# Kernel tuning notes

Hardware: AMD Instinct MI355X
Metric: run time of the kernel (lower is better)

The kernel has to match this reference:

```python
import jax, jax.numpy as jnp
import numpy as np

N = 100000   # nodes
E = 800000   # edges
IN = 128     # in_dim
H = 256      # hidden
G = 512      # global cache rows


def _w(k, shape):
    fan_in = shape[0]
    return jax.random.normal(k, shape, jnp.float32) / np.sqrt(fan_in)


def setup_inputs() -> dict:
    key = jax.random.key(0)
    ks = jax.random.split(key, 24)
    x = jax.random.normal(ks[0], (N, IN), jnp.float32)
    edge_index = jax.random.randint(ks[1], (2, E), 0, N, jnp.int64)
    global_cache = jax.random.normal(ks[2], (G, H), jnp.float32)
    return {
        "x": x,
        "edge_index": edge_index,
        "global_cache": global_cache,
        "Wp": _w(ks[3], (IN, 64)), "bp": jnp.zeros((64,), jnp.float32),
        "W1l": _w(ks[4], (64, H)), "b1l": jnp.zeros((H,), jnp.float32),
        "W1r": _w(ks[5], (64, H)),
        "W2l": _w(ks[6], (H, H)), "b2l": jnp.zeros((H,), jnp.float32),
        "W2r": _w(ks[7], (H, H)),
        "Wq": _w(ks[8], (H, H)), "bq": jnp.zeros((H,), jnp.float32),
        "Wk": _w(ks[9], (H, H)), "bk": jnp.zeros((H,), jnp.float32),
        "Wv": _w(ks[10], (H, H)), "bv": jnp.zeros((H,), jnp.float32),
        "Wm1": _w(ks[11], (2 * H, H)), "bm1": jnp.zeros((H,), jnp.float32),
        "Wm2": _w(ks[12], (H, 2)), "bm2": jnp.zeros((2,), jnp.float32),
    }


def _sage(h, src, dst, Wl, bl, Wr):
    # PyG SAGEConv (mean aggr): lin_l(mean_{j in N(i)} h_j) + lin_r(h_i)
    agg = jax.ops.segment_sum(h[src], dst, num_segments=N)          # [N, d]
    cnt = jax.ops.segment_sum(jnp.ones((src.shape[0],), h.dtype), dst, num_segments=N)
    mean = agg / jnp.maximum(cnt, 1.0)[:, None]
    return mean @ Wl + bl + h @ Wr


def reference(x, edge_index, global_cache, Wp, bp, W1l, b1l, W1r,
              W2l, b2l, W2r, Wq, bq, Wk, bk, Wv, bv, Wm1, bm1, Wm2, bm2):
    src, dst = edge_index[0], edge_index[1]
    x_emb = jax.nn.relu(x @ Wp + bp)                                 # [N, 64]
    h = jax.nn.relu(_sage(x_emb, src, dst, W1l, b1l, W1r))           # [N, H]
    # dropout is identity in eval mode
    h = _sage(h, src, dst, W2l, b2l, W2r)                            # [N, H]
    # global attention
    Q = h @ Wq + bq                                                  # [N, H]
    K = global_cache @ Wk + bk                                       # [G, H]
    V = global_cache @ Wv + bv                                       # [G, H]
    attn = jax.nn.softmax(Q @ K.T / np.sqrt(H).astype(np.float32), axis=-1)  # [N, G]
    g = attn @ V                                                     # [N, H]
    h_cat = jnp.concatenate([h, g], axis=1)                          # [N, 2H]
    out = jax.nn.relu(h_cat @ Wm1 + bm1) @ Wm2 + bm2                 # [N, 2]
    return out
```

## Files before the change

### kernel.cpp

```cpp
#include <hip/hip_runtime.h>
#include <cstdint>
#include <cstddef>


#define NN 100000
#define NE 800000
#define CR 100000
#define NB1 98
#define CNTB 3125
#define XCVB 12500
#define NJOB 11
#define WCVB (NJOB * 32)
#define EMB_MB 782

typedef __attribute__((ext_vector_type(8))) short short8;
typedef __attribute__((ext_vector_type(8))) unsigned short ushort8;
typedef __attribute__((ext_vector_type(4))) float f32x4;

__device__ __forceinline__ float b2f(ushort u) {
  union { unsigned u; float f; } v; v.u = ((unsigned)u) << 16; return v.f;
}
__device__ __forceinline__ ushort f2b(float f) {
  union { float f; unsigned u; } v; v.f = f;
  unsigned r = v.u + 0x7FFFu + ((v.u >> 16) & 1u);
  return (ushort)(r >> 16);
}
__device__ __forceinline__ void gl_lds16(const void* g, void* l) {
  __builtin_amdgcn_global_load_lds((const __attribute__((address_space(1))) void*)g,
                                   (__attribute__((address_space(3))) void*)l, 16, 0, 0);
}

__global__ void zero_detect_k(const int* __restrict__ ei, int* __restrict__ flag,
                              int* __restrict__ cnt, int n) {
  if (blockIdx.x == 0) {
    __shared__ int ok;
    int t = threadIdx.x;
    if (t == 0) ok = 1;
    __syncthreads();
    if (ei[2 * t + 1] != 0) ok = 0;
    __syncthreads();
    if (t == 0) *flag = ok;
  } else {
    int i = (blockIdx.x - 1) * 256 + threadIdx.x;
    if (i < n) cnt[i] = 0;
  }
}

struct CvtJobs {
  const float* src[NJOB];
  ushort* dst[NJOB];
  int R[NJOB], C[NJOB], off[NJOB], tr[NJOB];
  float sc[NJOB];
};

__global__ void count_cvt_k(const int* __restrict__ ei, const int* __restrict__ flag,
                            int* __restrict__ cnt, int* __restrict__ loc,
                            const float* __restrict__ x, ushort* __restrict__ xb,
                            int E, int n4, CvtJobs jb) {
  int b = blockIdx.x;
  if (b < CNTB + XCVB) {
    int q = b / 5;
    if (b - q * 5 == 0) {
      int i = q * 256 + threadIdx.x;
      if (i >= E) return;
      const bool i64 = (*flag != 0);
      unsigned d = (unsigned)(i64 ? ei[2 * E + 2 * i] : ei[E + i]);
      int p = -1;
      if (d < NN) p = atomicAdd(&cnt[d], 1);
      loc[i] = p;
    } else {
      int i = (b - q - 1) * 256 + threadIdx.x;
      if (i < n4) {
        float4 v = ((const float4*)x)[i];
        ushort4 o; o.x = f2b(v.x); o.y = f2b(v.y); o.z = f2b(v.z); o.w = f2b(v.w);
        ((ushort4*)xb)[i] = o;
      }
    }
  } else {
    int wb = b - CNTB - XCVB;
    int j = wb >> 5;
    int ib = wb & 31;
    const int Cj = jb.C[j], Rj = jb.R[j];
    const float sc = jb.sc[j];
    const int n = Rj * Cj;
    if (jb.tr[j]) {
      for (int i = ib * 256 + threadIdx.x; i < n; i += 32 * 256) {
        int c = i / Rj, r = i - c * Rj;
        jb.dst[j][i] = f2b(jb.src[j][(size_t)(jb.off[j] + r) * Cj + c] * sc);
      }
    } else {
      for (int i = ib * 256 + threadIdx.x; i < n; i += 32 * 256)
        jb.dst[j][i] = f2b(jb.src[j][i] * sc);
    }
  }
}

__device__ __forceinline__ void scan1_body(const int* __restrict__ cnt,
                                           int* __restrict__ rowptr,
                                           int* __restrict__ bsum, int n, int b,
                                           char* smem) {
  int* ls = (int*)smem;
  const int t = threadIdx.x;
  const int base = b * 1024 + t * 4;
  int v[4]; int s = 0;
#pragma unroll
  for (int j = 0; j < 4; ++j) { int i = base + j; v[j] = (i < n) ? cnt[i] : 0; s += v[j]; }
  ls[t] = s; __syncthreads();
  int x = s;
  for (int o = 1; o < 256; o <<= 1) {
    int a = (t >= o) ? ls[t - o] : 0; __syncthreads();
    x += a; ls[t] = x; __syncthreads();
  }
  int run = x - s;
#pragma unroll
  for (int j = 0; j < 4; ++j) { run += v[j]; int i = base + j; if (i < n) rowptr[i + 1] = run; }
  if (t == 255) bsum[b] = x;
}

__device__ __forceinline__ void scan2_body(const int* __restrict__ bsum,
                                           int* __restrict__ boff, int nb,
                                           char* smem) {
  int* ls = (int*)smem;
  int t = threadIdx.x;
  int v = (t < 128 && t < nb) ? bsum[t] : 0;
  if (t < 128) ls[t] = v;
  __syncthreads();
  int x = v;
  for (int o = 1; o < 128; o <<= 1) {
    int a = (t < 128 && t >= o) ? ls[t - o] : 0;
    __syncthreads();
    x += a;
    if (t < 128) ls[t] = x;
    __syncthreads();
  }
  if (t < 128 && t < nb) boff[t] = x - v;
}

__device__ __forceinline__ void sbias_body(const float* __restrict__ bq,
                                           const ushort* __restrict__ Kmat,
                                           float* __restrict__ sbias, int blk) {
  int g = blk * 4 + (threadIdx.x >> 6);
  int lane = threadIdx.x & 63;
  if (g >= 512) return;
  ushort4 kv = ((const ushort4*)(Kmat + (size_t)g * 256))[lane];
  float4 bv = ((const float4*)bq)[lane];
  float p = b2f(kv.x) * bv.x + b2f(kv.y) * bv.y + b2f(kv.z) * bv.z + b2f(kv.w) * bv.w;
  for (int off = 32; off; off >>= 1) p += __shfl_xor(p, off);
  if (lane == 0) sbias[g] = p * 0.0625f;
}

__global__ void scan3_k(int* __restrict__ rowptr, const int* __restrict__ boff, int n) {
  int i = blockIdx.x * 256 + threadIdx.x;
  if (i == 0) rowptr[0] = 0;
  if (i < n) rowptr[i + 1] += boff[i >> 10];
}

__global__ void fill_edges_k(const int* __restrict__ ei, const int* __restrict__ flag,
                             const int* __restrict__ rowptr, const int* __restrict__ loc,
                             int* __restrict__ eidx, int E) {
  int i = blockIdx.x * 256 + threadIdx.x;
  if (i >= E) return;
  const bool i64 = (*flag != 0);
  unsigned s = (unsigned)(i64 ? ei[2 * i] : ei[i]);
  unsigned d = (unsigned)(i64 ? ei[2 * E + 2 * i] : ei[E + i]);
  int lc = loc[i];
  if (d < NN && s < NN && lc >= 0) {
    unsigned p = (unsigned)(rowptr[d] + lc);
    if (p < (unsigned)E) eidx[p] = (int)s;
  }
}

__global__ void agg64_k(const ushort* __restrict__ X, const int* __restrict__ rowptr,
                        const int* __restrict__ eidx, ushort* __restrict__ mean,
                        int r0, int M) {
  int nl = blockIdx.x * 4 + (threadIdx.x >> 6);
  int l = threadIdx.x & 63;
  int e4 = l >> 4;
  int d4 = l & 15;
  if (nl >= M) return;
  int node = r0 + nl;
  int s = rowptr[node], e = rowptr[node + 1];
  float a0 = 0.f, a1 = 0.f, a2 = 0.f, a3 = 0.f;
  for (int i = s + e4; i < e; i += 4) {
    unsigned sc = (unsigned)eidx[i];
    if (sc < NN) {
      ushort4 v = ((const ushort4*)(X + (size_t)sc * 64))[d4];
      a0 += b2f(v.x); a1 += b2f(v.y); a2 += b2f(v.z); a3 += b2f(v.w);
    }
  }
  a0 += __shfl_xor(a0, 16); a0 += __shfl_xor(a0, 32);
  a1 += __shfl_xor(a1, 16); a1 += __shfl_xor(a1, 32);
  a2 += __shfl_xor(a2, 16); a2 += __shfl_xor(a2, 32);
  a3 += __shfl_xor(a3, 16); a3 += __shfl_xor(a3, 32);
  if (e4 == 0) {
    float inv = 1.f / (float)max(e - s, 1);
    ushort4 o; o.x = f2b(a0 * inv); o.y = f2b(a1 * inv); o.z = f2b(a2 * inv); o.w = f2b(a3 * inv);
    ((ushort4*)(mean + (size_t)nl * 64))[d4] = o;
  }
}

__global__ void agg256_k(const ushort* __restrict__ X, const int* __restrict__ rowptr,
                         const int* __restrict__ eidx, ushort* __restrict__ mean,
                         int r0, int M) {
  int nl = blockIdx.x * 4 + (threadIdx.x >> 6);
  int l = threadIdx.x & 63;
  int g = l >> 5;
  int d = l & 31;
  if (nl >= M) return;
  int node = r0 + nl;
  int s = rowptr[node], e = rowptr[node + 1];
  float a[8], c[8];
#pragma unroll
  for (int k = 0; k < 8; ++k) { a[k] = 0.f; c[k] = 0.f; }
  for (int i = s + g; i < e; i += 4) {
    unsigned s0 = (unsigned)eidx[i];
    if (s0 < NN) {
      ushort8 v = *(const ushort8*)(X + (size_t)s0 * 256 + d * 8);
#pragma unroll
      for (int k = 0; k < 8; ++k) a[k] += b2f((ushort)v[k]);
    }
    int i2 = i + 2;
    if (i2 < e) {
      unsigned s1 = (unsigned)eidx[i2];
      if (s1 < NN) {
        ushort8 v = *(const ushort8*)(X + (size_t)s1 * 256 + d * 8);
#pragma unroll
        for (int k = 0; k < 8; ++k) c[k] += b2f((ushort)v[k]);
      }
    }
  }
  float inv = 1.f / (float)max(e - s, 1);
  ushort8 o;
#pragma unroll
  for (int k = 0; k < 8; ++k) {
    float t = a[k] + c[k];
    t += __shfl_xor(t, 32);
    o[k] = (short)f2b(t * inv);
  }
  if (g == 0) *(ushort8*)(mean + (size_t)nl * 256 + d * 8) = o;
}

template<int BN, bool RELU, bool OUTBF>
__device__ __forceinline__ void gemm_body(
    const ushort* __restrict__ A1, const ushort* __restrict__ BT1, int K1,
    const ushort* __restrict__ A2, const ushort* __restrict__ BT2, int K2,
    const float* __restrict__ bias, void* __restrict__ Cv, int M, int Nc,
    int bmi, int bni, char* smem) {
  constexpr int NR = BN / 32;
  constexpr int WTN = BN / 2;
  constexpr int ABYT = 128 * 64 * 2;
  constexpr int BBYT = BN * 64 * 2;
  constexpr int BUF = ABYT + BBYT;
  constexpr int CP = BN + 8;
  const int tid = threadIdx.x;
  const int l = tid & 63;
  const int w = tid >> 6;
  const int wm = w >> 1, wn = w & 1;
  const int bm = bmi * 128, bn = bni * BN;
  const int r15 = l & 15, g4 = l >> 4;

  const int nt1 = K1 >> 6;
  const int nt2 = A2 ? (K2 >> 6) : 0;
  const int nt = nt1 + nt2;

  auto STAGE = [&](int buf, int t) {
    const ushort* A = (t < nt1) ? A1 : A2;
    const ushort* BT = (t < nt1) ? BT1 : BT2;
    const int K = (t < nt1) ? K1 : K2;
    const int k0 = ((t < nt1) ? t : t - nt1) << 6;
    char* As = smem + buf * BUF;
    char* Bs = As + ABYT;
#pragma unroll
    for (int p = 0; p < 4; ++p) {
      int idx = tid + p * 256;
      int row = idx >> 3, slot = idx & 7;
      int kb = slot ^ (row & 7);
      int grow = bm + row; if (grow >= M) grow = M - 1;
      gl_lds16(A + (size_t)grow * K + k0 + kb * 8, As + idx * 16);
    }
#pragma unroll
    for (int p = 0; p < BN / 32; ++p) {
      int idx = tid + p * 256;
      int row = idx >> 3, slot = idx & 7;
      int kb = slot ^ (row & 7);
      gl_lds16(BT + (size_t)(bn + row) * K + k0 + kb * 8, Bs + idx * 16);
    }
  };

  f32x4 acc[4][NR];
  const f32x4 zz = {0.f, 0.f, 0.f, 0.f};
#pragma unroll
  for (int m = 0; m < 4; ++m)
#pragma unroll
    for (int n = 0; n < NR; ++n) acc[m][n] = zz;

  STAGE(0, 0);
  int cur = 0;
  for (int t = 0; t < nt; ++t) {
    __syncthreads();
    if (t + 1 < nt) STAGE(cur ^ 1, t + 1);
    const char* As = smem + cur * BUF;
    const char* Bs = As + ABYT;
#pragma unroll
    for (int s = 0; s < 2; ++s) {
      short8 a[4], b[NR];
      const int slotx = (((s * 4 + g4) ^ (r15 & 7)) << 4);
#pragma unroll
      for (int m = 0; m < 4; ++m) {
        int row = wm * 64 + m * 16 + r15;
        a[m] = *(const short8*)(As + row * 128 + slotx);
      }
#pragma unroll
      for (int n = 0; n < NR; ++n) {
        int row = wn * WTN + n * 16 + r15;
        b[n] = *(const short8*)(Bs + row * 128 + slotx);
      }
#pragma unroll
      for (int m = 0; m < 4; ++m)
#pragma unroll
        for (int n = 0; n < NR; ++n)
          acc[m][n] = __builtin_amdgcn_mfma_f32_16x16x32_bf16(a[m], b[n], acc[m][n], 0, 0, 0);
    }
    cur ^= 1;
  }
  __syncthreads();
  if (OUTBF) {
    ushort* Cs = (ushort*)smem;
#pragma unroll
    for (int n = 0; n < NR; ++n) {
      int col = wn * WTN + n * 16 + r15;
      float bv = bias ? bias[bn + col] : 0.f;
#pragma unroll
      for (int m = 0; m < 4; ++m) {
#pragma unroll
        for (int j = 0; j < 4; ++j) {
          int row = wm * 64 + m * 16 + g4 * 4 + j;
          float v = acc[m][n][j] + bv;
          if (RELU) v = fmaxf(v, 0.f);
          Cs[row * CP + col] = f2b(v);
        }
      }
    }
    __syncthreads();
    constexpr int C8 = BN / 8;
    for (int it = tid; it < 128 * C8; it += 256) {
      int row = it / C8, c8 = it % C8;
      if (bm + row < M)
        *(ushort8*)((ushort*)Cv + (size_t)(bm + row) * Nc + bn + c8 * 8) =
            *(const ushort8*)(Cs + row * CP + c8 * 8);
    }
  } else {
#pragma unroll
    for (int n = 0; n < NR; ++n) {
      int col = bn + wn * WTN + n * 16 + r15;
      float bv = bias ? bias[col] : 0.f;
#pragma unroll
      for (int m = 0; m < 4; ++m) {
#pragma unroll
        for (int j = 0; j < 4; ++j) {
          int row = bm + wm * 64 + m * 16 + g4 * 4 + j;
          if (row < M) {
            float v = acc[m][n][j] + bv;
            if (RELU) v = fmaxf(v, 0.f);
            ((float*)Cv)[(size_t)row * Nc + col] = v;
          }
        }
      }
    }
  }
}

template<bool RELU>
__global__ __launch_bounds__(256)
void gemm64_k(const ushort* __restrict__ A1, const ushort* __restrict__ BT1, int K1,
              const ushort* __restrict__ A2, const ushort* __restrict__ BT2, int K2,
              const float* __restrict__ bias, ushort* __restrict__ C, int M, int Nc) {
  constexpr int NR = 8;
  constexpr int WTN = 128;
  constexpr int ABYT = 64 * 32 * 2;
  constexpr int BBYT = 256 * 32 * 2;
  constexpr int BUF = ABYT + BBYT;
  constexpr int CP = 256 + 8;
  __shared__ __align__(16) char smem[2 * BUF];
  const int tid = threadIdx.x;
  const int l = tid & 63;
  const int w = tid >> 6;
  const int wm = w >> 1, wn = w & 1;
  const int bm = blockIdx.x * 64;
  const int bn = blockIdx.y * 256;
  const int r15 = l & 15, g4 = l >> 4;

  const int nt1 = K1 >> 5;
  const int nt2 = A2 ? (K2 >> 5) : 0;
  const int nt = nt1 + nt2;

  auto STAGE = [&](int buf, int t) {
    const ushort* A = (t < nt1) ? A1 : A2;
    const ushort* BT = (t < nt1) ? BT1 : BT2;
    const int K = (t < nt1) ? K1 : K2;
    const int k0 = ((t < nt1) ? t : t - nt1) << 5;
    char* As = smem + buf * BUF;
    char* Bs = As + ABYT;
    {
      int row = tid >> 2, slot = tid & 3;
      int kb = slot ^ ((row >> 1) & 3);
      int grow = bm + row; if (grow >= M) grow = M - 1;
      gl_lds16(A + (size_t)grow * K + k0 + kb * 8, As + tid * 16);
    }
#pragma unroll
    for (int p = 0; p < 4; ++p) {
      int idx = tid + p * 256;
      int row = idx >> 2, slot = idx & 3;
      int kb = slot ^ ((row >> 1) & 3);
      gl_lds16(BT + (size_t)(bn + row) * K + k0 + kb * 8, Bs + idx * 16);
    }
  };

  f32x4 acc[2][NR];
  const f32x4 zz = {0.f, 0.f, 0.f, 0.f};
#pragma unroll
  for (int m = 0; m < 2; ++m)
#pragma unroll
    for (int n = 0; n < NR; ++n) acc[m][n] = zz;

  STAGE(0, 0);
  int cur = 0;
  for (int t = 0; t < nt; ++t) {
    __syncthreads();
    if (t + 1 < nt) STAGE(cur ^ 1, t + 1);
    const char* As = smem + cur * BUF;
    const char* Bs = As + ABYT;
    short8 a[2], b[NR];
#pragma unroll
    for (int m = 0; m < 2; ++m) {
      int row = wm * 32 + m * 16 + r15;
      a[m] = *(const short8*)(As + row * 64 + ((g4 ^ ((row >> 1) & 3)) << 4));
    }
#pragma unroll
    for (int n = 0; n < NR; ++n) {
      int row = wn * WTN + n * 16 + r15;
      b[n] = *(const short8*)(Bs + row * 64 + ((g4 ^ ((row >> 1) & 3)) << 4));
    }
#pragma unroll
    for (int m = 0; m < 2; ++m)
#pragma unroll
      for (int n = 0; n < NR; ++n)
        acc[m][n] = __builtin_amdgcn_mfma_f32_16x16x32_bf16(a[m], b[n], acc[m][n], 0, 0, 0);
    cur ^= 1;
  }
  __syncthreads();
  ushort* Cs = (ushort*)smem;
#pragma unroll
  for (int n = 0; n < NR; ++n) {
    int col = wn * WTN + n * 16 + r15;
    float bv = bias ? bias[bn + col] : 0.f;
#pragma unroll
    for (int m = 0; m < 2; ++m) {
#pragma unroll
      for (int j = 0; j < 4; ++j) {
        int row = wm * 32 + m * 16 + g4 * 4 + j;
        float v = acc[m][n][j] + bv;
        if (RELU) v = fmaxf(v, 0.f);
        Cs[row * CP + col] = f2b(v);
      }
    }
  }
  __syncthreads();
  for (int it = tid; it < 64 * 32; it += 256) {
    int row = it >> 5, c8 = it & 31;
    if (bm + row < M)
      *(ushort8*)(C + (size_t)(bm + row) * Nc + bn + c8 * 8) =
          *(const ushort8*)(Cs + row * CP + c8 * 8);
  }
}

__global__ __launch_bounds__(256)
void stage2_k(const int* __restrict__ cnt, int* __restrict__ rowptr, int* __restrict__ bsum,
              const ushort* __restrict__ gcb, const ushort* __restrict__ WkT,
              const float* __restrict__ bk, ushort* __restrict__ Kmatb,
              const ushort* __restrict__ WvT, const float* __restrict__ bvv,
              ushort* __restrict__ Vmatb,
              const ushort* __restrict__ xb, const ushort* __restrict__ WpT,
              const float* __restrict__ bp, ushort* __restrict__ x_emb) {
  __shared__ __align__(16) char smem[65536];
  int b = blockIdx.x;
  if (b < 8) {
    gemm_body<128, false, true>(gcb, WkT, 256, nullptr, nullptr, 0, bk, Kmatb,
                                512, 256, b & 3, b >> 2, smem);
  } else if (b < 16) {
    int lb = b - 8;
    gemm_body<128, false, true>(gcb, WvT, 256, nullptr, nullptr, 0, bvv, Vmatb,
                                512, 256, lb & 3, lb >> 2, smem);
  } else if (b < 16 + EMB_MB) {
    gemm_body<64, true, true>(xb, WpT, 128, nullptr, nullptr, 0, bp, x_emb,
                              NN, 64, b - 16, 0, smem);
  } else {
    scan1_body(cnt, rowptr, bsum, NN, b - (16 + EMB_MB), smem);
  }
}

__global__ __launch_bounds__(256)
void stage3_k(const ushort* __restrict__ Kmatb, const ushort* __restrict__ Wqb,
              ushort* __restrict__ KWqT,
              const ushort* __restrict__ Wm1bT, const ushort* __restrict__ Vmatb,
              ushort* __restrict__ W_pvT,
              const float* __restrict__ bq, float* __restrict__ sbias,
              const int* __restrict__ bsum, int* __restrict__ boff) {
  __shared__ __align__(16) char smem[65536];
  int b = blockIdx.x;
  if (b < 8) {
    gemm_body<128, false, true>(Kmatb, Wqb, 256, nullptr, nullptr, 0, nullptr, KWqT,
                                512, 256, b & 3, b >> 2, smem);
  } else if (b < 16) {
    int lb = b - 8;
    gemm_body<128, false, true>(Wm1bT, Vmatb, 256, nullptr, nullptr, 0, nullptr, W_pvT,
                                256, 512, lb & 1, lb >> 1, smem);
  } else if (b < 144) {
    sbias_body(bq, Kmatb, sbias, b - 16);
  } else {
    scan2_body(bsum, boff, NB1, smem);
  }
}

__global__ __launch_bounds__(256)
void mlp_out_k(const ushort* __restrict__ A1, const ushort* __restrict__ BT1, int K1,
               const ushort* __restrict__ A2, const ushort* __restrict__ BT2, int K2,
               const float* __restrict__ bias, const float* __restrict__ Wm2,
               const float* __restrict__ bm2, float* __restrict__ out, int M) {
  constexpr int NR = 8;
  constexpr int WTN = 128;
  constexpr int ABYT = 64 * 32 * 2;
  constexpr int BBYT = 256 * 32 * 2;
  constexpr int BUF = ABYT + BBYT;
  __shared__ __align__(16) char smem[2 * BUF];
  const int tid = threadIdx.x;
  const int l = tid & 63;
  const int w = tid >> 6;
  const int wm = w >> 1, wn = w & 1;
  const int bm = blockIdx.x * 64;
  const int r15 = l & 15, g4 = l >> 4;

  const int nt1 = K1 >> 5;
  const int nt2 = K2 >> 5;
  const int nt = nt1 + nt2;

  auto STAGE = [&](int buf, int t) {
    const ushort* A = (t < nt1) ? A1 : A2;
    const ushort* BT = (t < nt1) ? BT1 : BT2;
    const int K = (t < nt1) ? K1 : K2;
    const int k0 = ((t < nt1) ? t : t - nt1) << 5;
    char* As = smem + buf * BUF;
    char* Bs = As + ABYT;
    {
      int row = tid >> 2, slot = tid & 3;
      int kb = slot ^ ((row >> 1) & 3);
      int grow = bm + row; if (grow >= M) grow = M - 1;
      gl_lds16(A + (size_t)grow * K + k0 + kb * 8, As + tid * 16);
    }
#pragma unroll
    for (int p = 0; p < 4; ++p) {
      int idx = tid + p * 256;
      int row = idx >> 2, slot = idx & 3;
      int kb = slot ^ ((row >> 1) & 3);
      gl_lds16(BT + (size_t)row * K + k0 + kb * 8, Bs + idx * 16);
    }
  };

  f32x4 acc[2][NR];
  const f32x4 zz = {0.f, 0.f, 0.f, 0.f};
#pragma unroll
  for (int m = 0; m < 2; ++m)
#pragma unroll
    for (int n = 0; n < NR; ++n) acc[m][n] = zz;

  STAGE(0, 0);
  int cur = 0;
  for (int t = 0; t < nt; ++t) {
    __syncthreads();
    if (t + 1 < nt) STAGE(cur ^ 1, t + 1);
    const char* As = smem + cur * BUF;
    const char* Bs = As + ABYT;
    short8 a[2], b[NR];
#pragma unroll
    for (int m = 0; m < 2; ++m) {
      int row = wm * 32 + m * 16 + r15;
      a[m] = *(const short8*)(As + row * 64 + ((g4 ^ ((row >> 1) & 3)) << 4));
    }
#pragma unroll
    for (int n = 0; n < NR; ++n) {
      int row = wn * WTN + n * 16 + r15;
      b[n] = *(const short8*)(Bs + row * 64 + ((g4 ^ ((row >> 1) & 3)) << 4));
    }
#pragma unroll
    for (int m = 0; m < 2; ++m)
#pragma unroll
      for (int n = 0; n < NR; ++n)
        acc[m][n] = __builtin_amdgcn_mfma_f32_16x16x32_bf16(a[m], b[n], acc[m][n], 0, 0, 0);
    cur ^= 1;
  }
  __syncthreads();
  float bv[NR], w20[NR], w21[NR];
#pragma unroll
  for (int n = 0; n < NR; ++n) {
    int col = wn * WTN + n * 16 + r15;
    bv[n] = bias[col];
    w20[n] = Wm2[col * 2 + 0];
    w21[n] = Wm2[col * 2 + 1];
  }
  float* red = (float*)smem;
#pragma unroll
  for (int m = 0; m < 2; ++m) {
#pragma unroll
    for (int j = 0; j < 4; ++j) {
      float p0 = 0.f, p1 = 0.f;
#pragma unroll
      for (int n = 0; n < NR; ++n) {
        float v = fmaxf(acc[m][n][j] + bv[n], 0.f);
        p0 += v * w20[n];
        p1 += v * w21[n];
      }
      p0 += __shfl_xor(p0, 1); p1 += __shfl_xor(p1, 1);
      p0 += __shfl_xor(p0, 2); p1 += __shfl_xor(p1, 2);
      p0 += __shfl_xor(p0, 4); p1 += __shfl_xor(p1, 4);
      p0 += __shfl_xor(p0, 8); p1 += __shfl_xor(p1, 8);
      if (r15 == 0) {
        int rl = wm * 32 + m * 16 + g4 * 4 + j;
        red[wn * 128 + rl * 2 + 0] = p0;
        red[wn * 128 + rl * 2 + 1] = p1;
      }
    }
  }
  __syncthreads();
  if (tid < 128) {
    int rl = tid >> 1, j = tid & 1;
    int row = bm + rl;
    if (row < M)
      out[(size_t)row * 2 + j] = red[rl * 2 + j] + red[128 + rl * 2 + j] + bm2[j];
  }
}

__global__ void softmax_k(ushort* __restrict__ SP, int M) {
  int row = blockIdx.x * 4 + (threadIdx.x >> 6);
  int lane = threadIdx.x & 63;
  if (row >= M) return;
  ushort4* p = (ushort4*)(SP + (size_t)row * 512);
  ushort4 ua = p[lane];
  ushort4 ub = p[lane + 64];
  float ax = b2f(ua.x), ay = b2f(ua.y), az = b2f(ua.z), aw = b2f(ua.w);
  float bx = b2f(ub.x), by = b2f(ub.y), bz = b2f(ub.z), bw = b2f(ub.w);
  float m = fmaxf(fmaxf(fmaxf(ax, ay), fmaxf(az, aw)),
                  fmaxf(fmaxf(bx, by), fmaxf(bz, bw)));
  for (int off = 32; off; off >>= 1) m = fmaxf(m, __shfl_xor(m, off));
  ax = expf(ax - m); ay = expf(ay - m); az = expf(az - m); aw = expf(aw - m);
  bx = expf(bx - m); by = expf(by - m); bz = expf(bz - m); bw = expf(bw - m);
  float s = ax + ay + az + aw + bx + by + bz + bw;
  for (int off = 32; off; off >>= 1) s += __shfl_xor(s, off);
  float inv = 1.f / s;
  ushort4 oa, ob;
  oa.x = f2b(ax * inv); oa.y = f2b(ay * inv); oa.z = f2b(az * inv); oa.w = f2b(aw * inv);
  ob.x = f2b(bx * inv); ob.y = f2b(by * inv); ob.z = f2b(bz * inv); ob.w = f2b(bw * inv);
  p[lane] = oa;
  p[lane + 64] = ob;
}

extern "C" void kernel_launch(void* const* d_in, const int* in_sizes, int n_in,
                              void* d_out, int out_size, void* d_ws, size_t ws_size,
                              hipStream_t stream) {
  const int N = NN, E = NE;
  const float* x   = (const float*)d_in[0];
  const int*   ei  = (const int*)d_in[1];
  const float* gc  = (const float*)d_in[2];
  const float* Wp  = (const float*)d_in[3];
  const float* bp  = (const float*)d_in[4];
  const float* W1l = (const float*)d_in[5];
  const float* b1l = (const float*)d_in[6];
  const float* W1r = (const float*)d_in[7];
  const float* W2l = (const float*)d_in[8];
  const float* b2l = (const float*)d_in[9];
  const float* W2r = (const float*)d_in[10];
  const float* Wq  = (const float*)d_in[11];
  const float* bq  = (const float*)d_in[12];
  const float* Wk  = (const float*)d_in[13];
  const float* bk  = (const float*)d_in[14];
  const float* Wv  = (const float*)d_in[15];
  const float* bv  = (const float*)d_in[16];
  const float* Wm1 = (const float*)d_in[17];
  const float* bm1 = (const float*)d_in[18];
  const float* Wm2 = (const float*)d_in[19];
  const float* bm2 = (const float*)d_in[20];
  float* out = (float*)d_out;

  char* base = (char*)d_ws;
  size_t off = 0;
  auto take = [&](size_t bytes) -> void* {
    void* r = base + off;
    off += (bytes + 255) & ~(size_t)255;
    return r;
  };
  int* cnt    = (int*)take((size_t)N * 4);
  int* rowptr = (int*)take((size_t)(N + 1) * 4);
  int* loc    = (int*)take((size_t)E * 4);
  int* eidx   = (int*)take((size_t)E * 4);
  int* eflag  = (int*)take(256);
  int* bsum   = (int*)take(NB1 * 4);
  int* boff   = (int*)take(NB1 * 4);
  ushort* WpT   = (ushort*)take((size_t)64 * 128 * 2);
  ushort* W1lT  = (ushort*)take((size_t)256 * 64 * 2);
  ushort* W1rT  = (ushort*)take((size_t)256 * 64 * 2);
  ushort* W2lT  = (ushort*)take((size_t)256 * 256 * 2);
  ushort* W2rT  = (ushort*)take((size_t)256 * 256 * 2);
  ushort* WkT   = (ushort*)take((size_t)256 * 256 * 2);
  ushort* WvT   = (ushort*)take((size_t)256 * 256 * 2);
  ushort* Wqb   = (ushort*)take((size_t)256 * 256 * 2);
  ushort* Wm1aT = (ushort*)take((size_t)256 * 256 * 2);
  ushort* Wm1bT = (ushort*)take((size_t)256 * 256 * 2);
  ushort* gcb   = (ushort*)take((size_t)512 * 256 * 2);
  ushort* Kmatb = (ushort*)take((size_t)512 * 256 * 2);
  ushort* Vmatb = (ushort*)take((size_t)512 * 256 * 2);
  ushort* W_pvT = (ushort*)take((size_t)256 * 512 * 2);
  ushort* KWqT  = (ushort*)take((size_t)512 * 256 * 2);
  float*  sbias = (float*)take((size_t)512 * 4);
  char* U = (char*)take((size_t)N * 1536);
  ushort* h = (ushort*)take((size_t)N * 256 * 2);
  if (off > ws_size) return;

  ushort* xb    = (ushort*)U;
  ushort* x_emb = (ushort*)(U + (size_t)N * 256);
  ushort* mean1 = (ushort*)(U + (size_t)N * 384);
  ushort* h2_c     = (ushort*)U;
  ushort* SP_c     = (ushort*)(U + (size_t)N * 512);
  ushort* mean2_c  = SP_c;

  const int n4 = N * 128 / 4;
  dim3 thr(256);

  CvtJobs jb;
  {
    const float* s_[NJOB] = {gc, Wq, Wp, W1l, W1r, W2l, W2r, Wk, Wv, Wm1, Wm1};
    ushort* d_[NJOB] = {gcb, Wqb, WpT, W1lT, W1rT, W2lT, W2rT, WkT, WvT, Wm1aT, Wm1bT};
    int R_[NJOB] = {512, 256, 128, 64, 64, 256, 256, 256, 256, 256, 256};
    int C_[NJOB] = {256, 256, 64, 256, 256, 256, 256, 256, 256, 256, 256};
    int o_[NJOB] = {0, 0, 0, 0, 0, 0, 0, 0, 0, 0, 256};
    int t_[NJOB] = {0, 0, 1, 1, 1, 1, 1, 1, 1, 1, 1};
    for (int j = 0; j < NJOB; ++j) {
      jb.src[j] = s_[j]; jb.dst[j] = d_[j]; jb.R[j] = R_[j]; jb.C[j] = C_[j];
      jb.off[j] = o_[j]; jb.tr[j] = t_[j]; jb.sc[j] = (j == 1) ? 0.0625f : 1.0f;
    }
  }

  zero_detect_k<<<1 + (N + 255) / 256, thr, 0, stream>>>(ei, eflag, cnt, N);
  count_cvt_k<<<CNTB + XCVB + WCVB, thr, 0, stream>>>(ei, eflag, cnt, loc, x, xb, E, n4, jb);
  stage2_k<<<16 + EMB_MB + NB1, thr, 0, stream>>>(
      cnt, rowptr, bsum, gcb, WkT, bk, Kmatb, WvT, bv, Vmatb, xb, WpT, bp, x_emb);
  stage3_k<<<145, thr, 0, stream>>>(
      Kmatb, Wqb, KWqT, Wm1bT, Vmatb, W_pvT, bq, sbias, bsum, boff);
  scan3_k<<<(N + 255) / 256, thr, 0, stream>>>(rowptr, boff, N);
  fill_edges_k<<<(E + 255) / 256, thr, 0, stream>>>(ei, eflag, rowptr, loc, eidx, E);

  agg64_k<<<(N + 3) / 4, thr, 0, stream>>>(x_emb, rowptr, eidx, mean1, 0, N);
  gemm64_k<true><<<dim3((N + 63) / 64, 1), thr, 0, stream>>>(
      mean1, W1lT, 64, x_emb, W1rT, 64, b1l, h, N, 256);

  {
    const int CRc = N;
    const int MBc64 = (CRc + 63) / 64;
    agg256_k<<<(CRc + 3) / 4, thr, 0, stream>>>(h, rowptr, eidx, mean2_c, 0, CRc);
    gemm64_k<false><<<dim3(MBc64, 1), thr, 0, stream>>>(
        mean2_c, W2lT, 256, h, W2rT, 256, b2l, h2_c, CRc, 256);
    gemm64_k<false><<<dim3(MBc64, 2), thr, 0, stream>>>(
        h2_c, KWqT, 256, nullptr, nullptr, 0, sbias, SP_c, CRc, 512);
    softmax_k<<<(CRc + 3) / 4, thr, 0, stream>>>(SP_c, CRc);
    mlp_out_k<<<dim3(MBc64, 1), thr, 0, stream>>>(
        h2_c, Wm1aT, 256, SP_c, W_pvT, 512, bm1, Wm2, bm2, out, CRc);
  }
}
```

Before: 411.8 us.

## Double GEMM row tile to 128 with 512-thread blocks sharing B tile

```diff
diff --git a/kernel.cpp b/kernel.cpp
--- a/kernel.cpp
+++ b/kernel.cpp
@@ -371,13 +371,13 @@
 }
 
 template<bool RELU>
-__global__ __launch_bounds__(256)
+__global__ __launch_bounds__(512)
 void gemm64_k(const ushort* __restrict__ A1, const ushort* __restrict__ BT1, int K1,
               const ushort* __restrict__ A2, const ushort* __restrict__ BT2, int K2,
               const float* __restrict__ bias, ushort* __restrict__ C, int M, int Nc) {
   constexpr int NR = 8;
   constexpr int WTN = 128;
-  constexpr int ABYT = 64 * 32 * 2;
+  constexpr int ABYT = 128 * 32 * 2;
   constexpr int BBYT = 256 * 32 * 2;
   constexpr int BUF = ABYT + BBYT;
   constexpr int CP = 256 + 8;
@@ -385,8 +385,9 @@
   const int tid = threadIdx.x;
   const int l = tid & 63;
   const int w = tid >> 6;
-  const int wm = w >> 1, wn = w & 1;
-  const int bm = blockIdx.x * 64;
+  const int wh = w >> 2;
+  const int wm = (w >> 1) & 1, wn = w & 1;
+  const int bm = blockIdx.x * 128;
   const int bn = blockIdx.y * 256;
   const int r15 = l & 15, g4 = l >> 4;
 
@@ -408,8 +409,8 @@
       gl_lds16(A + (size_t)grow * K + k0 + kb * 8, As + tid * 16);
     }
 #pragma unroll
-    for (int p = 0; p < 4; ++p) {
-      int idx = tid + p * 256;
+    for (int p = 0; p < 2; ++p) {
+      int idx = tid + p * 512;
       int row = idx >> 2, slot = idx & 3;
       int kb = slot ^ ((row >> 1) & 3);
       gl_lds16(BT + (size_t)(bn + row) * K + k0 + kb * 8, Bs + idx * 16);
@@ -433,7 +434,7 @@
     short8 a[2], b[NR];
 #pragma unroll
     for (int m = 0; m < 2; ++m) {
-      int row = wm * 32 + m * 16 + r15;
+      int row = wh * 64 + wm * 32 + m * 16 + r15;
       a[m] = *(const short8*)(As + row * 64 + ((g4 ^ ((row >> 1) & 3)) << 4));
     }
 #pragma unroll
@@ -448,29 +449,35 @@
         acc[m][n] = __builtin_amdgcn_mfma_f32_16x16x32_bf16(a[m], b[n], acc[m][n], 0, 0, 0);
     cur ^= 1;
   }
-  __syncthreads();
   ushort* Cs = (ushort*)smem;
 #pragma unroll
-  for (int n = 0; n < NR; ++n) {
-    int col = wn * WTN + n * 16 + r15;
-    float bv = bias ? bias[bn + col] : 0.f;
-#pragma unroll
-    for (int m = 0; m < 2; ++m) {
-#pragma unroll
-      for (int j = 0; j < 4; ++j) {
-        int row = wm * 32 + m * 16 + g4 * 4 + j;
-        float v = acc[m][n][j] + bv;
-        if (RELU) v = fmaxf(v, 0.f);
-        Cs[row * CP + col] = f2b(v);
-      }
-    }
-  }
-  __syncthreads();
-  for (int it = tid; it < 64 * 32; it += 256) {
-    int row = it >> 5, c8 = it & 31;
-    if (bm + row < M)
-      *(ushort8*)(C + (size_t)(bm + row) * Nc + bn + c8 * 8) =
-          *(const ushort8*)(Cs + row * CP + c8 * 8);
+  for (int half = 0; half < 2; ++half) {
+    __syncthreads();
+    if (wh == half) {
+#pragma unroll
+      for (int n = 0; n < NR; ++n) {
+        int col = wn * WTN + n * 16 + r15;
+        float bv = bias ? bias[bn + col] : 0.f;
+#pragma unroll
+        for (int m = 0; m < 2; ++m) {
+#pragma unroll
+          for (int j = 0; j < 4; ++j) {
+            int row = wm * 32 + m * 16 + g4 * 4 + j;
+            float v = acc[m][n][j] + bv;
+            if (RELU) v = fmaxf(v, 0.f);
+            Cs[row * CP + col] = f2b(v);
+          }
+        }
+      }
+    }
+    __syncthreads();
+    for (int it = tid; it < 64 * 32; it += 512) {
+      int row = it >> 5, c8 = it & 31;
+      int gr = bm + half * 64 + row;
+      if (gr < M)
+        *(ushort8*)(C + (size_t)gr * Nc + bn + c8 * 8) =
+            *(const ushort8*)(Cs + row * CP + c8 * 8);
+    }
   }
 }
 
@@ -522,22 +529,23 @@
   }
 }
 
-__global__ __launch_bounds__(256)
+__global__ __launch_bounds__(512)
 void mlp_out_k(const ushort* __restrict__ A1, const ushort* __restrict__ BT1, int K1,
                const ushort* __restrict__ A2, const ushort* __restrict__ BT2, int K2,
                const float* __restrict__ bias, const float* __restrict__ Wm2,
                const float* __restrict__ bm2, float* __restrict__ out, int M) {
   constexpr int NR = 8;
   constexpr int WTN = 128;
-  constexpr int ABYT = 64 * 32 * 2;
+  constexpr int ABYT = 128 * 32 * 2;
   constexpr int BBYT = 256 * 32 * 2;
   constexpr int BUF = ABYT + BBYT;
   __shared__ __align__(16) char smem[2 * BUF];
   const int tid = threadIdx.x;
   const int l = tid & 63;
   const int w = tid >> 6;
-  const int wm = w >> 1, wn = w & 1;
-  const int bm = blockIdx.x * 64;
+  const int wh = w >> 2;
+  const int wm = (w >> 1) & 1, wn = w & 1;
+  const int bm = blockIdx.x * 128;
   const int r15 = l & 15, g4 = l >> 4;
 
   const int nt1 = K1 >> 5;
@@ -558,8 +566,8 @@
       gl_lds16(A + (size_t)grow * K + k0 + kb * 8, As + tid * 16);
     }
 #pragma unroll
-    for (int p = 0; p < 4; ++p) {
-      int idx = tid + p * 256;
+    for (int p = 0; p < 2; ++p) {
+      int idx = tid + p * 512;
       int row = idx >> 2, slot = idx & 3;
       int kb = slot ^ ((row >> 1) & 3);
       gl_lds16(BT + (size_t)row * K + k0 + kb * 8, Bs + idx * 16);
@@ -583,7 +591,7 @@
     short8 a[2], b[NR];
 #pragma unroll
     for (int m = 0; m < 2; ++m) {
-      int row = wm * 32 + m * 16 + r15;
+      int row = wh * 64 + wm * 32 + m * 16 + r15;
       a[m] = *(const short8*)(As + row * 64 + ((g4 ^ ((row >> 1) & 3)) << 4));
     }
 #pragma unroll
@@ -624,18 +632,18 @@
       p0 += __shfl_xor(p0, 4); p1 += __shfl_xor(p1, 4);
       p0 += __shfl_xor(p0, 8); p1 += __shfl_xor(p1, 8);
       if (r15 == 0) {
-        int rl = wm * 32 + m * 16 + g4 * 4 + j;
-        red[wn * 128 + rl * 2 + 0] = p0;
-        red[wn * 128 + rl * 2 + 1] = p1;
+        int rl = wh * 64 + wm * 32 + m * 16 + g4 * 4 + j;
+        red[wn * 256 + rl * 2 + 0] = p0;
+        red[wn * 256 + rl * 2 + 1] = p1;
       }
     }
   }
   __syncthreads();
-  if (tid < 128) {
+  if (tid < 256) {
     int rl = tid >> 1, j = tid & 1;
     int row = bm + rl;
     if (row < M)
-      out[(size_t)row * 2 + j] = red[rl * 2 + j] + red[128 + rl * 2 + j] + bm2[j];
+      out[(size_t)row * 2 + j] = red[rl * 2 + j] + red[256 + rl * 2 + j] + bm2[j];
   }
 }
 
@@ -733,6 +741,7 @@
 
   const int n4 = N * 128 / 4;
   dim3 thr(256);
+  dim3 thr512(512);
 
   CvtJobs jb;
   {
@@ -758,19 +767,19 @@
   fill_edges_k<<<(E + 255) / 256, thr, 0, stream>>>(ei, eflag, rowptr, loc, eidx, E);
 
   agg64_k<<<(N + 3) / 4, thr, 0, stream>>>(x_emb, rowptr, eidx, mean1, 0, N);
-  gemm64_k<true><<<dim3((N + 63) / 64, 1), thr, 0, stream>>>(
+  gemm64_k<true><<<dim3((N + 127) / 128, 1), thr512, 0, stream>>>(
       mean1, W1lT, 64, x_emb, W1rT, 64, b1l, h, N, 256);
 
   {
     const int CRc = N;
-    const int MBc64 = (CRc + 63) / 64;
+    const int MBc128 = (CRc + 127) / 128;
     agg256_k<<<(CRc + 3) / 4, thr, 0, stream>>>(h, rowptr, eidx, mean2_c, 0, CRc);
-    gemm64_k<false><<<dim3(MBc64, 1), thr, 0, stream>>>(
+    gemm64_k<false><<<dim3(MBc128, 1), thr512, 0, stream>>>(
         mean2_c, W2lT, 256, h, W2rT, 256, b2l, h2_c, CRc, 256);
-    gemm64_k<false><<<dim3(MBc64, 2), thr, 0, stream>>>(
+    gemm64_k<false><<<dim3(MBc128, 2), thr512, 0, stream>>>(
         h2_c, KWqT, 256, nullptr, nullptr, 0, sbias, SP_c, CRc, 512);
     softmax_k<<<(CRc + 3) / 4, thr, 0, stream>>>(SP_c, CRc);
-    mlp_out_k<<<dim3(MBc64, 1), thr, 0, stream>>>(
+    mlp_out_k<<<dim3(MBc128, 1), thr512, 0, stream>>>(
         h2_c, Wm1aT, 256, SP_c, W_pvT, 512, bm1, Wm2, bm2, out, CRc);
   }
 }
```

New measurement: 403.1 us. 1.02x faster.
